# Optimization experiments

Measured on AMD Instinct MI355X. Metric: run time of the kernel, lower is better.

Reference implementation:

```python
import jax, jax.numpy as jnp
import numpy as np

NNK = 16
DENSITY_WEIGHT = 1.0


def _sq_dist(x, y):
    # x: [B, Nx, C], y: [B, Ny, C] -> [B, Nx, Ny] squared L2 distances.
    # Matmul form of the original broadcast-diff computation (same math,
    # avoids materializing [B, Nx, C, Ny]); clamp tiny negatives from fp error.
    x2 = jnp.sum(x * x, axis=-1)               # [B, Nx]
    y2 = jnp.sum(y * y, axis=-1)               # [B, Ny]
    xy = jnp.einsum('bnc,bmc->bnm', x, y)      # [B, Nx, Ny]
    return jnp.maximum(x2[:, :, None] + y2[:, None, :] - 2.0 * xy, 0.0)


def _safe_sqrt(s):
    # sqrt with zero (instead of inf) gradient at s == 0; forward values exact.
    pos = s > 0
    return jnp.where(pos, jnp.sqrt(jnp.where(pos, s, 1.0)), 0.0)


def setup_inputs() -> dict:
    key = jax.random.key(0)
    k1, k2 = jax.random.split(key)
    B, N, C = 2, 8192, 3
    y_pred = jax.random.normal(k1, (B, N, C), dtype=jnp.float32)
    y_true = jax.random.normal(k2, (B, N, C), dtype=jnp.float32)
    return {"y_pred": y_pred, "y_true": y_true}


def reference(y_pred, y_true):
    # dist[b, i, j] = || y_true[b, i] - y_pred[b, j] ||
    dist = _safe_sqrt(_sq_dist(y_true, y_pred))            # [B, Nt, Np]
    minrow = jnp.min(dist, axis=2)                         # per true point
    mincol = jnp.min(dist, axis=1)                         # per pred point
    shape_loss = (jnp.mean(minrow) + jnp.mean(mincol)) / 2

    dist2 = _safe_sqrt(_sq_dist(y_true, y_true))           # [B, Nt, Nt]
    knndis, _ = jax.lax.top_k(-dist, NNK)                  # [B, Nt, k]
    knndis2, _ = jax.lax.top_k(-dist2, NNK)                # [B, Nt, k]
    density_loss = jnp.mean(jnp.abs(knndis - knndis2))

    data_loss = shape_loss + density_loss * DENSITY_WEIGHT
    return (data_loss, shape_loss, density_loss)
```

## Files before the change

kernel.cpp:

```cpp
#include <hip/hip_runtime.h>
#include <math.h>

#define NPTS 8192
#define NB 2
#define NROWS (NB * NPTS)
#define KNN 16
#define KC 6

#define GRID 32
#define NCELLS (GRID * GRID * GRID)
#define TOTCELLS (4 * NCELLS)
#define H 0.35f
#define RLO (-5.6f)
#define INVH (1.0f / H)
#define SCAN_BLOCKS 128
#define SEGCAP 132

__device__ __forceinline__ int cellof(float x) {
  int c = (int)floorf((x - RLO) * INVH);
  return min(max(c, 0), GRID - 1);
}

__device__ __forceinline__ float sqd3(float qx, float qy, float qz, float4 c) {
  float dx = qx - c.x, dy = qy - c.y, dz = qz - c.z;
  return fmaf(dx, dx, fmaf(dy, dy, dz * dz));
}

__device__ __forceinline__ int lanerank(unsigned long long mk) {
  return __builtin_amdgcn_mbcnt_hi((unsigned)(mk >> 32),
                                   __builtin_amdgcn_mbcnt_lo((unsigned)mk, 0));
}

template <int K>
__device__ __forceinline__ void insertK(float (&a)[K], float d) {
  if (d < a[K - 1]) {
    a[K - 1] = d;
#pragma unroll
    for (int k = K - 1; k > 0; --k) {
      float lo = fminf(a[k - 1], a[k]);
      a[k] = fmaxf(a[k - 1], a[k]);
      a[k - 1] = lo;
    }
  }
}

__device__ __forceinline__ float bitonic_sort64(float v, int lane) {
#pragma unroll
  for (int k = 2; k <= 64; k <<= 1) {
#pragma unroll
    for (int j = k >> 1; j >= 1; j >>= 1) {
      float o = __shfl_xor(v, j, 64);
      bool up = ((lane & k) == 0);
      bool lower = ((lane & j) == 0);
      float mn = fminf(v, o), mx = fmaxf(v, o);
      v = (up == lower) ? mn : mx;
    }
  }
  return v;
}

template <int K, int NEED>
__device__ void wave_grid_knn(int g, float qx, float qy, float qz,
                              const float4* __restrict__ sorted,
                              const unsigned* __restrict__ pack,
                              unsigned* sS, unsigned* sC, unsigned* sPre,
                              int lane, float (&a)[K], float& dmin,
                              int& cnt, float& bnd2) {
  const int cx = cellof(qx), cy = cellof(qy), cz = cellof(qz);
  float fx = fminf(qx - (RLO + cx * H), (RLO + (cx + 1) * H) - qx);
  float fy = fminf(qy - (RLO + cy * H), (RLO + (cy + 1) * H) - qy);
  float fz = fminf(qz - (RLO + cz * H), (RLO + (cz + 1) * H) - qz);
  const float fq = fminf(fx, fminf(fy, fz));
  const int base = g * NCELLS;
  for (int m = 0; m <= GRID; ++m) {
    const int zlo = max(cz - m, 0), zhi = min(cz + m, GRID - 1);
    const int ylo = max(cy - m, 0), yhi = min(cy + m, GRID - 1);
    const int xlo = max(cx - m, 0), xhi = min(cx + m, GRID - 1);
    const int ny = yhi - ylo + 1;
    const int nrows = (zhi - zlo + 1) * ny;
    for (int rb = 0; rb < nrows; rb += 64) {
      const int rho = rb + lane;
      const bool act = rho < nrows;
      const int rr = act ? rho : 0;
      const int z = zlo + rr / ny, y = ylo + rr % ny;
      const int dza = abs(z - cz), dya = abs(y - cy);
      const bool bdry = (dza == m) || (dya == m);
      unsigned stA = 0, cnA = 0, stB = 0, cnB = 0;
      const int rowbase = base + (z * GRID + y) * GRID;
      if (act) {
        if (bdry) {
          unsigned plo = pack[rowbase + xlo];
          unsigned phi = pack[rowbase + xhi];
          stA = plo >> 14;
          cnA = ((phi >> 14) + (phi & 16383u)) - stA;
        } else {
          int xl = cx - m, xr = cx + m;
          if (xl >= 0) { unsigned p = pack[rowbase + xl]; stA = p >> 14; cnA = p & 16383u; }
          if (xr < GRID) { unsigned p = pack[rowbase + xr]; stB = p >> 14; cnB = p & 16383u; }
        }
      }
      unsigned long long mA = __ballot(cnA > 0);
      unsigned long long mB = __ballot(cnB > 0);
      int nA = __popcll(mA);
      int nseg = nA + __popcll(mB);
      if (nseg == 0) continue;
      int slA = lanerank(mA), slB = nA + lanerank(mB);
      if (cnA > 0) { sS[slA] = stA; sC[slA] = cnA; }
      if (cnB > 0) { sS[slB] = stB; sC[slB] = cnB; }
      unsigned total = 0;
      for (int h = 0; h < 2; ++h) {
        int sl = h * 64 + lane;
        unsigned v = (sl < nseg) ? sC[sl] : 0u;
        unsigned inc = v;
#pragma unroll
        for (int s2 = 1; s2 < 64; s2 <<= 1) {
          unsigned t = __shfl_up(inc, s2, 64);
          if (lane >= s2) inc += t;
        }
        if (sl < nseg) sPre[sl] = total + inc - v;
        total += __shfl(inc, 63, 64);
        if (nseg <= 64) break;
      }
      int sh0 = (nseg > 1) ? (1 << (31 - __clz(nseg - 1))) : 0;
      for (unsigned cb = 0; cb < total; cb += 64) {
        unsigned c = cb + (unsigned)lane;
        bool cact = c < total;
        unsigned cc = cact ? c : (total - 1);
        int lo = 0;
        for (int sh = sh0; sh; sh >>= 1) {
          int mid = lo + sh;
          if (mid < nseg && sPre[mid] <= cc) lo = mid;
        }
        float4 p = sorted[sS[lo] + (cc - sPre[lo])];
        float d = cact ? sqd3(qx, qy, qz, p) : INFINITY;
        dmin = fminf(dmin, fmaxf(d, a[K - 1]));
        insertK(a, d);
      }
    }
    float bnd = fmaxf((float)m * H + fq, 0.0f) * 0.999f;
    bnd2 = bnd * bnd;
    int c = 0;
#pragma unroll
    for (int k = 0; k < K; ++k) c += (a[k] <= bnd2) ? 1 : 0;
#pragma unroll
    for (int s2 = 1; s2 < 64; s2 <<= 1) c += __shfl_xor(c, s2, 64);
    cnt = c;
    bool covered = (zlo == 0 && zhi == GRID - 1 && ylo == 0 && yhi == GRID - 1 &&
                    xlo == 0 && xhi == GRID - 1);
    if (c >= NEED || covered) break;
  }
}

__global__ __launch_bounds__(256) void count_kernel(
    const float* __restrict__ yp, const float* __restrict__ yt,
    unsigned* __restrict__ counts, int* __restrict__ pflat,
    unsigned* __restrict__ prank) {
  int t = blockIdx.x * 256 + threadIdx.x;
  const float* src;
  int g;
  if (t < NROWS) { src = yp + 3 * t; g = 2 * (t >> 13); }
  else { int u = t - NROWS; src = yt + 3 * u; g = 2 * (u >> 13) + 1; }
  int flat = g * NCELLS + (cellof(src[2]) * GRID + cellof(src[1])) * GRID + cellof(src[0]);
  unsigned r = atomicAdd(&counts[flat], 1u);
  pflat[t] = flat;
  prank[t] = r;
}

__global__ __launch_bounds__(1024) void scan1_kernel(
    const unsigned* __restrict__ counts, unsigned* __restrict__ partial,
    unsigned* __restrict__ aux) {
  __shared__ unsigned ws[16];
  const int t = threadIdx.x, lane = t & 63, wave = t >> 6;
  const int tid = blockIdx.x * 1024 + t;
  unsigned v = counts[tid];
  unsigned inc = v;
#pragma unroll
  for (int off = 1; off < 64; off <<= 1) {
    unsigned u = __shfl_up(inc, off, 64);
    if (lane >= off) inc += u;
  }
  if (lane == 63) ws[wave] = inc;
  __syncthreads();
  unsigned wex = 0;
  if (wave == 0) {
    unsigned o = (lane < 16) ? ws[lane] : 0u;
    unsigned wi = o;
#pragma unroll
    for (int off = 1; off < 16; off <<= 1) {
      unsigned u = __shfl_up(wi, off, 64);
      if (lane >= off) wi += u;
    }
    if (lane < 16) ws[lane] = wi - o;
  }
  __syncthreads();
  wex = ws[wave];
  partial[tid] = wex + inc - v;
  if (t == 1023) aux[blockIdx.x] = wex + inc;
}

__global__ __launch_bounds__(1024) void pack_kernel(
    const unsigned* __restrict__ counts, const unsigned* __restrict__ partial,
    const unsigned* __restrict__ aux, unsigned* __restrict__ pack) {
  __shared__ unsigned sa[2];
  const int t = threadIdx.x;
  if (t < 128) {
    unsigned v = (t < (int)blockIdx.x) ? aux[t] : 0u;
#pragma unroll
    for (int s = 1; s < 64; s <<= 1) v += __shfl_xor(v, s, 64);
    if ((t & 63) == 0) sa[t >> 6] = v;
  }
  __syncthreads();
  unsigned base = sa[0] + sa[1];
  int i = blockIdx.x * 1024 + t;
  pack[i] = ((partial[i] + base) << 14) | counts[i];
}

__global__ __launch_bounds__(256) void scatter_kernel(
    const float* __restrict__ yp, const float* __restrict__ yt,
    const unsigned* __restrict__ pack, const int* __restrict__ pflat,
    const unsigned* __restrict__ prank, float4* __restrict__ sorted) {
  int t = blockIdx.x * 256 + threadIdx.x;
  const float* src;
  int row;
  if (t < NROWS) { row = t; src = yp + 3 * t; }
  else { row = t - NROWS; src = yt + 3 * row; }
  unsigned pos = (pack[pflat[t]] >> 14) + prank[t];
  sorted[pos] = make_float4(src[0], src[1], src[2], __int_as_float(row));
}

__global__ __launch_bounds__(256) void query_kernel(
    const float4* __restrict__ sorted, const unsigned* __restrict__ pack,
    float* __restrict__ knnP, float* __restrict__ knnT,
    float* __restrict__ mincol_arr, unsigned* __restrict__ flags) {
  __shared__ unsigned sb[4][3][SEGCAP];
  __shared__ float cbw[4][64];
  const int wave = threadIdx.x >> 6, lane = threadIdx.x & 63;
  const int wid = blockIdx.x * 4 + wave;
  const int type = wid >> 14;
  const int qid = wid & 16383;
  const int b = qid >> 13;
  const int src_g = (type == 2) ? 2 * b : 2 * b + 1;
  const int tgt_g = (type == 0) ? 2 * b : 2 * b + 1;
  float4 e = sorted[src_g * NPTS + (qid & (NPTS - 1))];
  const int row = __float_as_int(e.w);
  unsigned* sS = sb[wave][0];
  unsigned* sC = sb[wave][1];
  unsigned* sP = sb[wave][2];
  float* cbuf = cbw[wave];
  if (type < 2) {
    float a[KC];
#pragma unroll
    for (int k = 0; k < KC; ++k) a[k] = INFINITY;
    float dmin = INFINITY, bnd2;
    int cnt;
    wave_grid_knn<KC, KNN>(tgt_g, e.x, e.y, e.z, sorted, pack, sS, sC, sP,
                           lane, a, dmin, cnt, bnd2);
    float tau;
    if (cnt >= KNN && cnt <= 64) {
      tau = bnd2;
    } else {
      float slm = bitonic_sort64(a[0], lane);
      tau = __shfl(slm, 15, 64);
    }
    int tot = 0;
    int idx[KC];
#pragma unroll
    for (int k = 0; k < KC; ++k) {
      unsigned long long mk = __ballot(a[k] <= tau);
      idx[k] = tot + lanerank(mk);
      tot += __popcll(mk);
    }
#pragma unroll
    for (int k = 0; k < KC; ++k)
      if (a[k] <= tau && idx[k] < 64) cbuf[idx[k]] = a[k];
    float v = (lane < tot) ? cbuf[lane] : INFINITY;
    v = bitonic_sort64(v, lane);
    float f15 = __shfl(v, 15, 64);
    bool bad = (tot > 64) || (__ballot(dmin <= f15) != 0ull);
    float* dst = (type == 0) ? knnP : knnT;
    if (lane < KNN) dst[row * KNN + lane] = sqrtf(v);
    if (lane == 0) flags[type * NROWS + row] = bad ? 1u : 0u;
  } else {
    float a1[1] = {INFINITY};
    float dmin = INFINITY, bnd2;
    int cnt;
    wave_grid_knn<1, 1>(tgt_g, e.x, e.y, e.z, sorted, pack, sS, sC, sP,
                        lane, a1, dmin, cnt, bnd2);
    float v = a1[0];
#pragma unroll
    for (int s = 1; s < 64; s <<= 1) v = fminf(v, __shfl_xor(v, s, 64));
    if (lane == 0) mincol_arr[row] = sqrtf(v);
  }
}

__device__ float exact16_rowlist(const float4* __restrict__ base,
                                 float qx, float qy, float qz, int lane) {
  float a[KNN];
#pragma unroll
  for (int k = 0; k < KNN; ++k) a[k] = INFINITY;
  for (int s = 0; s < NPTS / 64; ++s) {
    float d = sqd3(qx, qy, qz, base[s * 64 + lane]);
    insertK(a, d);
  }
  float res = INFINITY;
#pragma unroll 1
  for (int r = 0; r < KNN; ++r) {
    float v = a[0];
    int idx = lane;
#pragma unroll
    for (int s = 1; s < 64; s <<= 1) {
      float ov = __shfl_xor(v, s, 64);
      int oi = __shfl_xor(idx, s, 64);
      bool take = (ov < v) || (ov == v && oi < idx);
      v = take ? ov : v;
      idx = take ? oi : idx;
    }
    if (lane == r) res = v;
    if (lane == idx) {
#pragma unroll
      for (int k = 0; k < KNN - 1; ++k) a[k] = a[k + 1];
      a[KNN - 1] = INFINITY;
    }
  }
  return res;
}

__global__ __launch_bounds__(256) void combine_kernel(
    const float* __restrict__ yt, const float4* __restrict__ sorted,
    const unsigned* __restrict__ flags, float* __restrict__ knnP,
    float* __restrict__ knnT, const float* __restrict__ mincol_arr,
    double* __restrict__ pd) {
  __shared__ double s1[256], s2[256], s3[256];
  const int t = threadIdx.x, lane = t & 63, wave = t >> 6;
  const int row0 = blockIdx.x * 256;
  const int rbase = row0 + wave * 64;
  unsigned f0 = flags[rbase + lane];
  unsigned f1 = flags[NROWS + rbase + lane];
  unsigned long long m0 = __ballot(f0 != 0u);
  unsigned long long m1 = __ballot(f1 != 0u);
  while (m0) {
    int rr = __ffsll(m0) - 1; m0 &= m0 - 1;
    int row = rbase + rr;
    int bb = row >> 13;
    const float* q = yt + 3 * row;
    float s = exact16_rowlist(sorted + (size_t)(2 * bb) * NPTS, q[0], q[1], q[2], lane);
    if (lane < KNN) knnP[row * KNN + lane] = sqrtf(s);
  }
  while (m1) {
    int rr = __ffsll(m1) - 1; m1 &= m1 - 1;
    int row = rbase + rr;
    int bb = row >> 13;
    const float* q = yt + 3 * row;
    float s = exact16_rowlist(sorted + (size_t)(2 * bb + 1) * NPTS, q[0], q[1], q[2], lane);
    if (lane < KNN) knnT[row * KNN + lane] = sqrtf(s);
  }
  __syncthreads();
  const int row = row0 + t;
  float s = 0.0f;
#pragma unroll
  for (int k = 0; k < KNN; ++k)
    s += fabsf(knnP[row * KNN + k] - knnT[row * KNN + k]);
  s1[t] = (double)knnP[row * KNN];
  s2[t] = (double)mincol_arr[row];
  s3[t] = (double)s;
  __syncthreads();
  for (int off = 128; off > 0; off >>= 1) {
    if (t < off) { s1[t] += s1[t + off]; s2[t] += s2[t + off]; s3[t] += s3[t + off]; }
    __syncthreads();
  }
  if (t == 0) {
    pd[blockIdx.x * 3 + 0] = s1[0];
    pd[blockIdx.x * 3 + 1] = s2[0];
    pd[blockIdx.x * 3 + 2] = s3[0];
  }
}

__global__ __launch_bounds__(64) void finalize_kernel(
    const double* __restrict__ pd, float* __restrict__ out) {
  const int t = threadIdx.x;
  double a = pd[t * 3], b = pd[t * 3 + 1], c = pd[t * 3 + 2];
#pragma unroll
  for (int s = 32; s >= 1; s >>= 1) {
    a += __shfl_down(a, s, 64);
    b += __shfl_down(b, s, 64);
    c += __shfl_down(c, s, 64);
  }
  if (t == 0) {
    double shape = 0.5 * (a + b) / (double)NROWS;
    double dens = c / ((double)NROWS * KNN);
    out[0] = (float)(shape + dens);
    out[1] = (float)shape;
    out[2] = (float)dens;
  }
}

extern "C" void kernel_launch(void* const* d_in, const int* in_sizes, int n_in,
                              void* d_out, int out_size, void* d_ws, size_t ws_size,
                              hipStream_t stream) {
  (void)in_sizes; (void)n_in; (void)out_size; (void)ws_size;
  const float* yp = (const float*)d_in[0];
  const float* yt = (const float*)d_in[1];
  char* w = (char*)d_ws;
  unsigned* counts  = (unsigned*)w;  w += TOTCELLS * 4;
  unsigned* partial = (unsigned*)w;  w += TOTCELLS * 4;
  unsigned* aux     = (unsigned*)w;  w += 512;
  unsigned* pack    = (unsigned*)w;  w += TOTCELLS * 4;
  int*      pflat   = (int*)w;       w += 2 * NROWS * 4;
  unsigned* prank   = (unsigned*)w;  w += 2 * NROWS * 4;
  float4*   sorted  = (float4*)w;    w += 2 * NROWS * 16;
  float*    knnP    = (float*)w;     w += NROWS * KNN * 4;
  float*    knnT    = (float*)w;     w += NROWS * KNN * 4;
  float*    mincol  = (float*)w;     w += NROWS * 4;
  unsigned* flags   = (unsigned*)w;  w += 2 * NROWS * 4;
  double*   pd      = (double*)w;    w += 64 * 3 * 8;
  float* out = (float*)d_out;

  hipMemsetAsync(counts, 0, (size_t)TOTCELLS * 4, stream);
  count_kernel<<<2 * NROWS / 256, 256, 0, stream>>>(yp, yt, counts, pflat, prank);
  scan1_kernel<<<SCAN_BLOCKS, 1024, 0, stream>>>(counts, partial, aux);
  pack_kernel<<<SCAN_BLOCKS, 1024, 0, stream>>>(counts, partial, aux, pack);
  scatter_kernel<<<2 * NROWS / 256, 256, 0, stream>>>(yp, yt, pack, pflat, prank, sorted);
  query_kernel<<<3 * 16384 / 4, 256, 0, stream>>>(sorted, pack, knnP, knnT, mincol, flags);
  combine_kernel<<<64, 256, 0, stream>>>(yt, sorted, flags, knnP, knnT, mincol, pd);
  finalize_kernel<<<1, 64, 0, stream>>>(pd, out);
}
```

Measured before the change: 136.3 us.

## Share grid neighbor-cell gathering across query chunks within the same cell

```diff
diff --git a/kernel.cpp b/kernel.cpp
--- a/kernel.cpp
+++ b/kernel.cpp
@@ -16,6 +16,11 @@
 #define SCAN_BLOCKS 128
 #define SEGCAP 132
 
+#define QC 8
+#define CAP 1024
+#define NEED 192
+#define MAXCHUNK 8192
+
 __device__ __forceinline__ int cellof(float x) {
   int c = (int)floorf((x - RLO) * INVH);
   return min(max(c, 0), GRID - 1);
@@ -59,26 +64,136 @@
   return v;
 }
 
-template <int K, int NEED>
-__device__ void wave_grid_knn(int g, float qx, float qy, float qz,
-                              const float4* __restrict__ sorted,
-                              const unsigned* __restrict__ pack,
-                              unsigned* sS, unsigned* sC, unsigned* sPre,
-                              int lane, float (&a)[K], float& dmin,
-                              int& cnt, float& bnd2) {
-  const int cx = cellof(qx), cy = cellof(qy), cz = cellof(qz);
-  float fx = fminf(qx - (RLO + cx * H), (RLO + (cx + 1) * H) - qx);
-  float fy = fminf(qy - (RLO + cy * H), (RLO + (cy + 1) * H) - qy);
-  float fz = fminf(qz - (RLO + cz * H), (RLO + (cz + 1) * H) - qz);
-  const float fq = fminf(fx, fminf(fy, fz));
-  const int base = g * NCELLS;
+__global__ __launch_bounds__(256) void count_kernel(
+    const float* __restrict__ yp, const float* __restrict__ yt,
+    unsigned* __restrict__ counts, int* __restrict__ pflat,
+    unsigned* __restrict__ prank, unsigned* __restrict__ wcnt) {
+  if (blockIdx.x == 0 && threadIdx.x < 4) wcnt[threadIdx.x] = 0;
+  int t = blockIdx.x * 256 + threadIdx.x;
+  const float* src;
+  int g;
+  if (t < NROWS) { src = yp + 3 * t; g = 2 * (t >> 13); }
+  else { int u = t - NROWS; src = yt + 3 * u; g = 2 * (u >> 13) + 1; }
+  int flat = g * NCELLS + (cellof(src[2]) * GRID + cellof(src[1])) * GRID + cellof(src[0]);
+  unsigned r = atomicAdd(&counts[flat], 1u);
+  pflat[t] = flat;
+  prank[t] = r;
+}
+
+__global__ __launch_bounds__(1024) void scan1_kernel(
+    const unsigned* __restrict__ counts, unsigned* __restrict__ partial,
+    unsigned* __restrict__ aux) {
+  __shared__ unsigned ws[16];
+  const int t = threadIdx.x, lane = t & 63, wave = t >> 6;
+  const int tid = blockIdx.x * 1024 + t;
+  unsigned v = counts[tid];
+  unsigned inc = v;
+#pragma unroll
+  for (int off = 1; off < 64; off <<= 1) {
+    unsigned u = __shfl_up(inc, off, 64);
+    if (lane >= off) inc += u;
+  }
+  if (lane == 63) ws[wave] = inc;
+  __syncthreads();
+  unsigned wex = 0;
+  if (wave == 0) {
+    unsigned o = (lane < 16) ? ws[lane] : 0u;
+    unsigned wi = o;
+#pragma unroll
+    for (int off = 1; off < 16; off <<= 1) {
+      unsigned u = __shfl_up(wi, off, 64);
+      if (lane >= off) wi += u;
+    }
+    if (lane < 16) ws[lane] = wi - o;
+  }
+  __syncthreads();
+  wex = ws[wave];
+  partial[tid] = wex + inc - v;
+  if (t == 1023) aux[blockIdx.x] = wex + inc;
+}
+
+__global__ __launch_bounds__(1024) void pack_kernel(
+    const unsigned* __restrict__ counts, const unsigned* __restrict__ partial,
+    const unsigned* __restrict__ aux, unsigned* __restrict__ pack,
+    unsigned* __restrict__ wcnt, unsigned* __restrict__ wlist) {
+  __shared__ unsigned sa[2];
+  const int t = threadIdx.x;
+  if (t < 128) {
+    unsigned v = (t < (int)blockIdx.x) ? aux[t] : 0u;
+#pragma unroll
+    for (int s = 1; s < 64; s <<= 1) v += __shfl_xor(v, s, 64);
+    if ((t & 63) == 0) sa[t >> 6] = v;
+  }
+  __syncthreads();
+  unsigned base = sa[0] + sa[1];
+  int i = blockIdx.x * 1024 + t;
+  unsigned cnti = counts[i];
+  pack[i] = ((partial[i] + base) << 14) | cnti;
+  if (cnti > 0) {
+    int g = i >> 15;
+    unsigned cellw = (unsigned)(i & (NCELLS - 1));
+    unsigned nch = (cnti + QC - 1) / QC;
+    unsigned slot = atomicAdd(&wcnt[g], nch);
+    for (unsigned j = 0; j < nch; ++j)
+      wlist[g * MAXCHUNK + slot + j] = (cellw << 11) | j;
+  }
+}
+
+__global__ __launch_bounds__(256) void scatter_kernel(
+    const float* __restrict__ yp, const float* __restrict__ yt,
+    const unsigned* __restrict__ pack, const int* __restrict__ pflat,
+    const unsigned* __restrict__ prank, float4* __restrict__ sorted) {
+  int t = blockIdx.x * 256 + threadIdx.x;
+  const float* src;
+  int row;
+  if (t < NROWS) { row = t; src = yp + 3 * t; }
+  else { row = t - NROWS; src = yt + 3 * row; }
+  unsigned pos = (pack[pflat[t]] >> 14) + prank[t];
+  sorted[pos] = make_float4(src[0], src[1], src[2], __int_as_float(row));
+}
+
+__global__ __launch_bounds__(256) void query_kernel(
+    const float4* __restrict__ sorted, const unsigned* __restrict__ pack,
+    const unsigned* __restrict__ wcnt, const unsigned* __restrict__ wlist,
+    float* __restrict__ knnP, float* __restrict__ knnT,
+    float* __restrict__ mincol_arr, unsigned* __restrict__ flags) {
+  __shared__ unsigned sb[4][3][SEGCAP];
+  __shared__ unsigned short bufw[4][CAP];
+  __shared__ float4 qbw[4][QC];
+  __shared__ float cbw[4][64];
+  const int wave = threadIdx.x >> 6, lane = threadIdx.x & 63;
+  const int wid = blockIdx.x * 4 + wave;
+  const int seg = wid >> 13;
+  const int idx = wid & 8191;
+  const int b = seg / 3, task = seg % 3;
+  const int qg = (task == 2) ? 2 * b : 2 * b + 1;
+  const int tg = (task == 0) ? 2 * b : 2 * b + 1;
+  if ((unsigned)idx >= wcnt[qg]) return;
+  const unsigned e = wlist[qg * MAXCHUNK + idx];
+  const int cell = (int)(e >> 11);
+  const int qoff = (int)(e & 2047u) * QC;
+  const unsigned pc = pack[qg * NCELLS + cell];
+  const int cstart = (int)(pc >> 14);
+  const int ccnt = (int)(pc & 16383u);
+  const int nq = min(QC, ccnt - qoff);
+  if (lane < nq) qbw[wave][lane] = sorted[cstart + qoff + lane];
+  const int cx = cell & (GRID - 1), cy = (cell >> 5) & (GRID - 1), cz = cell >> 10;
+  unsigned* sS = sb[wave][0];
+  unsigned* sC = sb[wave][1];
+  unsigned* sP = sb[wave][2];
+  unsigned short* buf = bufw[wave];
+  float* cbuf = cbw[wave];
+
+  int bufcount = 0, M = 0;
+  bool overflow = false;
+  const int base = tg * NCELLS;
   for (int m = 0; m <= GRID; ++m) {
     const int zlo = max(cz - m, 0), zhi = min(cz + m, GRID - 1);
     const int ylo = max(cy - m, 0), yhi = min(cy + m, GRID - 1);
     const int xlo = max(cx - m, 0), xhi = min(cx + m, GRID - 1);
     const int ny = yhi - ylo + 1;
     const int nrows = (zhi - zlo + 1) * ny;
-    for (int rb = 0; rb < nrows; rb += 64) {
+    for (int rb = 0; rb < nrows && !overflow; rb += 64) {
       const int rho = rb + lane;
       const bool act = rho < nrows;
       const int rr = act ? rho : 0;
@@ -117,179 +232,108 @@
           unsigned t = __shfl_up(inc, s2, 64);
           if (lane >= s2) inc += t;
         }
-        if (sl < nseg) sPre[sl] = total + inc - v;
+        if (sl < nseg) sP[sl] = total + inc - v;
         total += __shfl(inc, 63, 64);
         if (nseg <= 64) break;
       }
       int sh0 = (nseg > 1) ? (1 << (31 - __clz(nseg - 1))) : 0;
       for (unsigned cb = 0; cb < total; cb += 64) {
         unsigned c = cb + (unsigned)lane;
-        bool cact = c < total;
-        unsigned cc = cact ? c : (total - 1);
-        int lo = 0;
-        for (int sh = sh0; sh; sh >>= 1) {
-          int mid = lo + sh;
-          if (mid < nseg && sPre[mid] <= cc) lo = mid;
+        if (c < total && (int)c + bufcount < CAP) {
+          int lo = 0;
+          for (int sh = sh0; sh; sh >>= 1) {
+            int mid = lo + sh;
+            if (mid < nseg && sP[mid] <= c) lo = mid;
+          }
+          buf[bufcount + (int)c] = (unsigned short)(sS[lo] + (c - sP[lo]));
         }
-        float4 p = sorted[sS[lo] + (cc - sPre[lo])];
-        float d = cact ? sqd3(qx, qy, qz, p) : INFINITY;
-        dmin = fminf(dmin, fmaxf(d, a[K - 1]));
-        insertK(a, d);
-      }
-    }
-    float bnd = fmaxf((float)m * H + fq, 0.0f) * 0.999f;
-    bnd2 = bnd * bnd;
-    int c = 0;
-#pragma unroll
-    for (int k = 0; k < K; ++k) c += (a[k] <= bnd2) ? 1 : 0;
-#pragma unroll
-    for (int s2 = 1; s2 < 64; s2 <<= 1) c += __shfl_xor(c, s2, 64);
-    cnt = c;
+      }
+      bufcount += (int)total;
+      if (bufcount > CAP) overflow = true;
+    }
+    if (overflow) break;
+    M = m;
     bool covered = (zlo == 0 && zhi == GRID - 1 && ylo == 0 && yhi == GRID - 1 &&
                     xlo == 0 && xhi == GRID - 1);
-    if (c >= NEED || covered) break;
-  }
-}
-
-__global__ __launch_bounds__(256) void count_kernel(
-    const float* __restrict__ yp, const float* __restrict__ yt,
-    unsigned* __restrict__ counts, int* __restrict__ pflat,
-    unsigned* __restrict__ prank) {
-  int t = blockIdx.x * 256 + threadIdx.x;
-  const float* src;
-  int g;
-  if (t < NROWS) { src = yp + 3 * t; g = 2 * (t >> 13); }
-  else { int u = t - NROWS; src = yt + 3 * u; g = 2 * (u >> 13) + 1; }
-  int flat = g * NCELLS + (cellof(src[2]) * GRID + cellof(src[1])) * GRID + cellof(src[0]);
-  unsigned r = atomicAdd(&counts[flat], 1u);
-  pflat[t] = flat;
-  prank[t] = r;
-}
-
-__global__ __launch_bounds__(1024) void scan1_kernel(
-    const unsigned* __restrict__ counts, unsigned* __restrict__ partial,
-    unsigned* __restrict__ aux) {
-  __shared__ unsigned ws[16];
-  const int t = threadIdx.x, lane = t & 63, wave = t >> 6;
-  const int tid = blockIdx.x * 1024 + t;
-  unsigned v = counts[tid];
-  unsigned inc = v;
-#pragma unroll
-  for (int off = 1; off < 64; off <<= 1) {
-    unsigned u = __shfl_up(inc, off, 64);
-    if (lane >= off) inc += u;
-  }
-  if (lane == 63) ws[wave] = inc;
-  __syncthreads();
-  unsigned wex = 0;
-  if (wave == 0) {
-    unsigned o = (lane < 16) ? ws[lane] : 0u;
-    unsigned wi = o;
-#pragma unroll
-    for (int off = 1; off < 16; off <<= 1) {
-      unsigned u = __shfl_up(wi, off, 64);
-      if (lane >= off) wi += u;
-    }
-    if (lane < 16) ws[lane] = wi - o;
-  }
-  __syncthreads();
-  wex = ws[wave];
-  partial[tid] = wex + inc - v;
-  if (t == 1023) aux[blockIdx.x] = wex + inc;
-}
-
-__global__ __launch_bounds__(1024) void pack_kernel(
-    const unsigned* __restrict__ counts, const unsigned* __restrict__ partial,
-    const unsigned* __restrict__ aux, unsigned* __restrict__ pack) {
-  __shared__ unsigned sa[2];
-  const int t = threadIdx.x;
-  if (t < 128) {
-    unsigned v = (t < (int)blockIdx.x) ? aux[t] : 0u;
-#pragma unroll
-    for (int s = 1; s < 64; s <<= 1) v += __shfl_xor(v, s, 64);
-    if ((t & 63) == 0) sa[t >> 6] = v;
-  }
-  __syncthreads();
-  unsigned base = sa[0] + sa[1];
-  int i = blockIdx.x * 1024 + t;
-  pack[i] = ((partial[i] + base) << 14) | counts[i];
-}
-
-__global__ __launch_bounds__(256) void scatter_kernel(
-    const float* __restrict__ yp, const float* __restrict__ yt,
-    const unsigned* __restrict__ pack, const int* __restrict__ pflat,
-    const unsigned* __restrict__ prank, float4* __restrict__ sorted) {
-  int t = blockIdx.x * 256 + threadIdx.x;
-  const float* src;
-  int row;
-  if (t < NROWS) { row = t; src = yp + 3 * t; }
-  else { row = t - NROWS; src = yt + 3 * row; }
-  unsigned pos = (pack[pflat[t]] >> 14) + prank[t];
-  sorted[pos] = make_float4(src[0], src[1], src[2], __int_as_float(row));
-}
-
-__global__ __launch_bounds__(256) void query_kernel(
-    const float4* __restrict__ sorted, const unsigned* __restrict__ pack,
-    float* __restrict__ knnP, float* __restrict__ knnT,
-    float* __restrict__ mincol_arr, unsigned* __restrict__ flags) {
-  __shared__ unsigned sb[4][3][SEGCAP];
-  __shared__ float cbw[4][64];
-  const int wave = threadIdx.x >> 6, lane = threadIdx.x & 63;
-  const int wid = blockIdx.x * 4 + wave;
-  const int type = wid >> 14;
-  const int qid = wid & 16383;
-  const int b = qid >> 13;
-  const int src_g = (type == 2) ? 2 * b : 2 * b + 1;
-  const int tgt_g = (type == 0) ? 2 * b : 2 * b + 1;
-  float4 e = sorted[src_g * NPTS + (qid & (NPTS - 1))];
-  const int row = __float_as_int(e.w);
-  unsigned* sS = sb[wave][0];
-  unsigned* sC = sb[wave][1];
-  unsigned* sP = sb[wave][2];
-  float* cbuf = cbw[wave];
-  if (type < 2) {
-    float a[KC];
-#pragma unroll
-    for (int k = 0; k < KC; ++k) a[k] = INFINITY;
-    float dmin = INFINITY, bnd2;
-    int cnt;
-    wave_grid_knn<KC, KNN>(tgt_g, e.x, e.y, e.z, sorted, pack, sS, sC, sP,
-                           lane, a, dmin, cnt, bnd2);
-    float tau;
-    if (cnt >= KNN && cnt <= 64) {
-      tau = bnd2;
+    if (covered || (m >= 1 && bufcount >= NEED)) break;
+  }
+
+  const float mh = (float)M * H;
+  for (int j = 0; j < nq; ++j) {
+    float4 q = qbw[wave][j];
+    const int row = __float_as_int(q.w);
+    float fx = fminf(q.x - (RLO + cx * H), (RLO + (cx + 1) * H) - q.x);
+    float fy = fminf(q.y - (RLO + cy * H), (RLO + (cy + 1) * H) - q.y);
+    float fz = fminf(q.z - (RLO + cz * H), (RLO + (cz + 1) * H) - q.z);
+    float fq = fminf(fx, fminf(fy, fz));
+    float bnd = fmaxf(mh + fq, 0.0f) * 0.999f;
+    float bnd2 = bnd * bnd;
+    if (task < 2) {
+      float a[KC];
+#pragma unroll
+      for (int k = 0; k < KC; ++k) a[k] = INFINITY;
+      float dmin = INFINITY;
+      bool act = lane < bufcount;
+      float4 p = sorted[act ? (int)buf[lane] : 0];
+      for (int cb = 0; cb < bufcount; cb += 64) {
+        int pos2 = cb + 64 + lane;
+        bool act2 = pos2 < bufcount;
+        float4 p2 = sorted[act2 ? (int)buf[pos2] : 0];
+        float d = act ? sqd3(q.x, q.y, q.z, p) : INFINITY;
+        dmin = fminf(dmin, fmaxf(d, a[KC - 1]));
+        insertK(a, d);
+        p = p2; act = act2;
+      }
+      int cntq = 0;
+#pragma unroll
+      for (int k = 0; k < KC; ++k) cntq += (a[k] <= bnd2) ? 1 : 0;
+#pragma unroll
+      for (int s2 = 1; s2 < 64; s2 <<= 1) cntq += __shfl_xor(cntq, s2, 64);
+      float tau;
+      if (cntq >= KNN && cntq <= 64) {
+        tau = bnd2;
+      } else {
+        float slm = bitonic_sort64(a[0], lane);
+        tau = __shfl(slm, 15, 64);
+      }
+      int tot = 0;
+      int idxk[KC];
+#pragma unroll
+      for (int k = 0; k < KC; ++k) {
+        unsigned long long mk = __ballot(a[k] <= tau);
+        idxk[k] = tot + lanerank(mk);
+        tot += __popcll(mk);
+      }
+#pragma unroll
+      for (int k = 0; k < KC; ++k)
+        if (a[k] <= tau && idxk[k] < 64) cbuf[idxk[k]] = a[k];
+      float v = (lane < tot) ? cbuf[lane] : INFINITY;
+      v = bitonic_sort64(v, lane);
+      float f15 = __shfl(v, 15, 64);
+      bool bad = overflow || (tot > 64) || (__ballot(dmin <= f15) != 0ull) ||
+                 (f15 > bnd2);
+      float* dst = (task == 0) ? knnP : knnT;
+      if (lane < KNN) dst[row * KNN + lane] = sqrtf(v);
+      if (lane == 0) flags[task * NROWS + row] = bad ? 1u : 0u;
     } else {
-      float slm = bitonic_sort64(a[0], lane);
-      tau = __shfl(slm, 15, 64);
-    }
-    int tot = 0;
-    int idx[KC];
-#pragma unroll
-    for (int k = 0; k < KC; ++k) {
-      unsigned long long mk = __ballot(a[k] <= tau);
-      idx[k] = tot + lanerank(mk);
-      tot += __popcll(mk);
-    }
-#pragma unroll
-    for (int k = 0; k < KC; ++k)
-      if (a[k] <= tau && idx[k] < 64) cbuf[idx[k]] = a[k];
-    float v = (lane < tot) ? cbuf[lane] : INFINITY;
-    v = bitonic_sort64(v, lane);
-    float f15 = __shfl(v, 15, 64);
-    bool bad = (tot > 64) || (__ballot(dmin <= f15) != 0ull);
-    float* dst = (type == 0) ? knnP : knnT;
-    if (lane < KNN) dst[row * KNN + lane] = sqrtf(v);
-    if (lane == 0) flags[type * NROWS + row] = bad ? 1u : 0u;
-  } else {
-    float a1[1] = {INFINITY};
-    float dmin = INFINITY, bnd2;
-    int cnt;
-    wave_grid_knn<1, 1>(tgt_g, e.x, e.y, e.z, sorted, pack, sS, sC, sP,
-                        lane, a1, dmin, cnt, bnd2);
-    float v = a1[0];
-#pragma unroll
-    for (int s = 1; s < 64; s <<= 1) v = fminf(v, __shfl_xor(v, s, 64));
-    if (lane == 0) mincol_arr[row] = sqrtf(v);
+      float v = INFINITY;
+      bool act = lane < bufcount;
+      float4 p = sorted[act ? (int)buf[lane] : 0];
+      for (int cb = 0; cb < bufcount; cb += 64) {
+        int pos2 = cb + 64 + lane;
+        bool act2 = pos2 < bufcount;
+        float4 p2 = sorted[act2 ? (int)buf[pos2] : 0];
+        if (act) v = fminf(v, sqd3(q.x, q.y, q.z, p));
+        p = p2; act = act2;
+      }
+#pragma unroll
+      for (int s2 = 1; s2 < 64; s2 <<= 1) v = fminf(v, __shfl_xor(v, s2, 64));
+      bool bad = overflow || (v > bnd2);
+      if (lane == 0) {
+        mincol_arr[row] = sqrtf(v);
+        flags[2 * NROWS + row] = bad ? 1u : 0u;
+      }
+    }
   }
 }
 
@@ -326,18 +370,20 @@
 }
 
 __global__ __launch_bounds__(256) void combine_kernel(
-    const float* __restrict__ yt, const float4* __restrict__ sorted,
-    const unsigned* __restrict__ flags, float* __restrict__ knnP,
-    float* __restrict__ knnT, const float* __restrict__ mincol_arr,
-    double* __restrict__ pd) {
+    const float* __restrict__ yp, const float* __restrict__ yt,
+    const float4* __restrict__ sorted, const unsigned* __restrict__ flags,
+    float* __restrict__ knnP, float* __restrict__ knnT,
+    float* __restrict__ mincol_arr, double* __restrict__ pd) {
   __shared__ double s1[256], s2[256], s3[256];
   const int t = threadIdx.x, lane = t & 63, wave = t >> 6;
   const int row0 = blockIdx.x * 256;
   const int rbase = row0 + wave * 64;
   unsigned f0 = flags[rbase + lane];
   unsigned f1 = flags[NROWS + rbase + lane];
+  unsigned f2 = flags[2 * NROWS + rbase + lane];
   unsigned long long m0 = __ballot(f0 != 0u);
   unsigned long long m1 = __ballot(f1 != 0u);
+  unsigned long long m2 = __ballot(f2 != 0u);
   while (m0) {
     int rr = __ffsll(m0) - 1; m0 &= m0 - 1;
     int row = rbase + rr;
@@ -353,6 +399,19 @@
     const float* q = yt + 3 * row;
     float s = exact16_rowlist(sorted + (size_t)(2 * bb + 1) * NPTS, q[0], q[1], q[2], lane);
     if (lane < KNN) knnT[row * KNN + lane] = sqrtf(s);
+  }
+  while (m2) {
+    int rr = __ffsll(m2) - 1; m2 &= m2 - 1;
+    int row = rbase + rr;
+    int bb = row >> 13;
+    const float* q = yp + 3 * row;
+    const float4* bp = sorted + (size_t)(2 * bb + 1) * NPTS;
+    float v = INFINITY;
+    for (int s = 0; s < NPTS / 64; ++s)
+      v = fminf(v, sqd3(q[0], q[1], q[2], bp[s * 64 + lane]));
+#pragma unroll
+    for (int s = 1; s < 64; s <<= 1) v = fminf(v, __shfl_xor(v, s, 64));
+    if (lane == 0) mincol_arr[row] = sqrtf(v);
   }
   __syncthreads();
   const int row = row0 + t;
@@ -411,16 +470,19 @@
   float*    knnP    = (float*)w;     w += NROWS * KNN * 4;
   float*    knnT    = (float*)w;     w += NROWS * KNN * 4;
   float*    mincol  = (float*)w;     w += NROWS * 4;
-  unsigned* flags   = (unsigned*)w;  w += 2 * NROWS * 4;
+  unsigned* flags   = (unsigned*)w;  w += 3 * NROWS * 4;
   double*   pd      = (double*)w;    w += 64 * 3 * 8;
+  unsigned* wcnt    = (unsigned*)w;  w += 64;
+  unsigned* wlist   = (unsigned*)w;  w += 4 * MAXCHUNK * 4;
   float* out = (float*)d_out;
 
   hipMemsetAsync(counts, 0, (size_t)TOTCELLS * 4, stream);
-  count_kernel<<<2 * NROWS / 256, 256, 0, stream>>>(yp, yt, counts, pflat, prank);
+  count_kernel<<<2 * NROWS / 256, 256, 0, stream>>>(yp, yt, counts, pflat, prank, wcnt);
   scan1_kernel<<<SCAN_BLOCKS, 1024, 0, stream>>>(counts, partial, aux);
-  pack_kernel<<<SCAN_BLOCKS, 1024, 0, stream>>>(counts, partial, aux, pack);
+  pack_kernel<<<SCAN_BLOCKS, 1024, 0, stream>>>(counts, partial, aux, pack, wcnt, wlist);
   scatter_kernel<<<2 * NROWS / 256, 256, 0, stream>>>(yp, yt, pack, pflat, prank, sorted);
-  query_kernel<<<3 * 16384 / 4, 256, 0, stream>>>(sorted, pack, knnP, knnT, mincol, flags);
-  combine_kernel<<<64, 256, 0, stream>>>(yt, sorted, flags, knnP, knnT, mincol, pd);
+  query_kernel<<<6 * 8192 / 4, 256, 0, stream>>>(sorted, pack, wcnt, wlist,
+                                                 knnP, knnT, mincol, flags);
+  combine_kernel<<<64, 256, 0, stream>>>(yp, yt, sorted, flags, knnP, knnT, mincol, pd);
   finalize_kernel<<<1, 64, 0, stream>>>(pd, out);
 }
```

Result: slower. 239.9 us (+75.9%).

## Batch up to three same-cell queries per wave via a cell-based work list

Applied to the files above, without the earlier changes.

```diff
diff --git a/kernel.cpp b/kernel.cpp
--- a/kernel.cpp
+++ b/kernel.cpp
@@ -16,6 +16,10 @@
 #define SCAN_BLOCKS 128
 #define SEGCAP 132
 
+#define QC 3
+#define WLCAP 49152
+#define QBLOCKS 2048
+
 __device__ __forceinline__ int cellof(float x) {
   int c = (int)floorf((x - RLO) * INVH);
   return min(max(c, 0), GRID - 1);
@@ -59,18 +63,22 @@
   return v;
 }
 
-template <int K, int NEED>
-__device__ void wave_grid_knn(int g, float qx, float qy, float qz,
-                              const float4* __restrict__ sorted,
-                              const unsigned* __restrict__ pack,
-                              unsigned* sS, unsigned* sC, unsigned* sPre,
-                              int lane, float (&a)[K], float& dmin,
-                              int& cnt, float& bnd2) {
-  const int cx = cellof(qx), cy = cellof(qy), cz = cellof(qz);
-  float fx = fminf(qx - (RLO + cx * H), (RLO + (cx + 1) * H) - qx);
-  float fy = fminf(qy - (RLO + cy * H), (RLO + (cy + 1) * H) - qy);
-  float fz = fminf(qz - (RLO + cz * H), (RLO + (cz + 1) * H) - qz);
-  const float fq = fminf(fx, fminf(fy, fz));
+template <int K, int NEEDQ>
+__device__ __forceinline__ void wave_grid_knn_q(
+    int g, int cx, int cy, int cz,
+    const float (&qx)[QC], const float (&qy)[QC], const float (&qz)[QC],
+    const float4* __restrict__ sorted, const unsigned* __restrict__ pack,
+    unsigned* sS, unsigned* sC, unsigned* sPre, int lane,
+    float (&a)[QC][K], float (&dminq)[QC], int (&cntq)[QC],
+    float (&bnd2q)[QC]) {
+  float fq[QC];
+#pragma unroll
+  for (int q = 0; q < QC; ++q) {
+    float fx = fminf(qx[q] - (RLO + cx * H), (RLO + (cx + 1) * H) - qx[q]);
+    float fy = fminf(qy[q] - (RLO + cy * H), (RLO + (cy + 1) * H) - qy[q]);
+    float fz = fminf(qz[q] - (RLO + cz * H), (RLO + (cz + 1) * H) - qz[q]);
+    fq[q] = fminf(fx, fminf(fy, fz));
+  }
   const int base = g * NCELLS;
   for (int m = 0; m <= GRID; ++m) {
     const int zlo = max(cz - m, 0), zhi = min(cz + m, GRID - 1);
@@ -132,29 +140,45 @@
           if (mid < nseg && sPre[mid] <= cc) lo = mid;
         }
         float4 p = sorted[sS[lo] + (cc - sPre[lo])];
-        float d = cact ? sqd3(qx, qy, qz, p) : INFINITY;
-        dmin = fminf(dmin, fmaxf(d, a[K - 1]));
-        insertK(a, d);
-      }
-    }
-    float bnd = fmaxf((float)m * H + fq, 0.0f) * 0.999f;
-    bnd2 = bnd * bnd;
-    int c = 0;
-#pragma unroll
-    for (int k = 0; k < K; ++k) c += (a[k] <= bnd2) ? 1 : 0;
-#pragma unroll
-    for (int s2 = 1; s2 < 64; s2 <<= 1) c += __shfl_xor(c, s2, 64);
-    cnt = c;
+#pragma unroll
+        for (int q = 0; q < QC; ++q) {
+          float d = cact ? sqd3(qx[q], qy[q], qz[q], p) : INFINITY;
+          dminq[q] = fminf(dminq[q], fmaxf(d, a[q][K - 1]));
+          insertK(a[q], d);
+        }
+      }
+    }
+#pragma unroll
+    for (int q = 0; q < QC; ++q) {
+      float bnd = fmaxf((float)m * H + fq[q], 0.0f) * 0.999f;
+      bnd2q[q] = bnd * bnd;
+    }
+    int cpA = 0, cpB = 0;
+#pragma unroll
+    for (int k = 0; k < K; ++k) {
+      cpA += (a[0][k] <= bnd2q[0] ? 1 : 0) + (a[1][k] <= bnd2q[1] ? 65536 : 0);
+      cpB += (a[2][k] <= bnd2q[2] ? 1 : 0);
+    }
+#pragma unroll
+    for (int s2 = 1; s2 < 64; s2 <<= 1) {
+      cpA += __shfl_xor(cpA, s2, 64);
+      cpB += __shfl_xor(cpB, s2, 64);
+    }
+    cntq[0] = cpA & 0xffff;
+    cntq[1] = cpA >> 16;
+    cntq[2] = cpB;
+    bool okall = (cntq[0] >= NEEDQ) && (cntq[1] >= NEEDQ) && (cntq[2] >= NEEDQ);
     bool covered = (zlo == 0 && zhi == GRID - 1 && ylo == 0 && yhi == GRID - 1 &&
                     xlo == 0 && xhi == GRID - 1);
-    if (c >= NEED || covered) break;
+    if (okall || covered) break;
   }
 }
 
 __global__ __launch_bounds__(256) void count_kernel(
     const float* __restrict__ yp, const float* __restrict__ yt,
     unsigned* __restrict__ counts, int* __restrict__ pflat,
-    unsigned* __restrict__ prank) {
+    unsigned* __restrict__ prank, unsigned* __restrict__ wcnt) {
+  if (blockIdx.x == 0 && threadIdx.x < 8) wcnt[threadIdx.x] = 0;
   int t = blockIdx.x * 256 + threadIdx.x;
   const float* src;
   int g;
@@ -200,7 +224,8 @@
 
 __global__ __launch_bounds__(1024) void pack_kernel(
     const unsigned* __restrict__ counts, const unsigned* __restrict__ partial,
-    const unsigned* __restrict__ aux, unsigned* __restrict__ pack) {
+    const unsigned* __restrict__ aux, unsigned* __restrict__ pack,
+    unsigned* __restrict__ wcnt, unsigned* __restrict__ wlist) {
   __shared__ unsigned sa[2];
   const int t = threadIdx.x;
   if (t < 128) {
@@ -212,7 +237,25 @@
   __syncthreads();
   unsigned base = sa[0] + sa[1];
   int i = blockIdx.x * 1024 + t;
-  pack[i] = ((partial[i] + base) << 14) | counts[i];
+  unsigned cnti = counts[i];
+  pack[i] = ((partial[i] + base) << 14) | cnti;
+  if (cnti > 0) {
+    int g = i >> 15;
+    unsigned b = (unsigned)(g >> 1);
+    unsigned cellw = (unsigned)(i & (NCELLS - 1));
+    unsigned nch = (cnti + QC - 1) / QC;
+    if (g & 1) {
+      unsigned slot = atomicAdd(&wcnt[4], 2 * nch);
+      for (unsigned j = 0; j < nch; ++j) {
+        wlist[slot + 2 * j]     = (b << 30) | (0u << 28) | (cellw << 13) | j;
+        wlist[slot + 2 * j + 1] = (b << 30) | (1u << 28) | (cellw << 13) | j;
+      }
+    } else {
+      unsigned slot = atomicAdd(&wcnt[4], nch);
+      for (unsigned j = 0; j < nch; ++j)
+        wlist[slot + j] = (b << 30) | (2u << 28) | (cellw << 13) | j;
+    }
+  }
 }
 
 __global__ __launch_bounds__(256) void scatter_kernel(
@@ -230,66 +273,101 @@
 
 __global__ __launch_bounds__(256) void query_kernel(
     const float4* __restrict__ sorted, const unsigned* __restrict__ pack,
+    const unsigned* __restrict__ wcnt, const unsigned* __restrict__ wlist,
     float* __restrict__ knnP, float* __restrict__ knnT,
     float* __restrict__ mincol_arr, unsigned* __restrict__ flags) {
   __shared__ unsigned sb[4][3][SEGCAP];
   __shared__ float cbw[4][64];
   const int wave = threadIdx.x >> 6, lane = threadIdx.x & 63;
-  const int wid = blockIdx.x * 4 + wave;
-  const int type = wid >> 14;
-  const int qid = wid & 16383;
-  const int b = qid >> 13;
-  const int src_g = (type == 2) ? 2 * b : 2 * b + 1;
-  const int tgt_g = (type == 0) ? 2 * b : 2 * b + 1;
-  float4 e = sorted[src_g * NPTS + (qid & (NPTS - 1))];
-  const int row = __float_as_int(e.w);
   unsigned* sS = sb[wave][0];
   unsigned* sC = sb[wave][1];
   unsigned* sP = sb[wave][2];
   float* cbuf = cbw[wave];
-  if (type < 2) {
-    float a[KC];
-#pragma unroll
-    for (int k = 0; k < KC; ++k) a[k] = INFINITY;
-    float dmin = INFINITY, bnd2;
-    int cnt;
-    wave_grid_knn<KC, KNN>(tgt_g, e.x, e.y, e.z, sorted, pack, sS, sC, sP,
-                           lane, a, dmin, cnt, bnd2);
-    float tau;
-    if (cnt >= KNN && cnt <= 64) {
-      tau = bnd2;
+  const unsigned nwork = wcnt[4];
+  const unsigned nw = gridDim.x * 4;
+  for (unsigned wrk = blockIdx.x * 4 + wave; wrk < nwork; wrk += nw) {
+    const unsigned e = wlist[wrk];
+    const int b = (int)((e >> 30) & 1u);
+    const int task = (int)((e >> 28) & 3u);
+    const int cell = (int)((e >> 13) & 32767u);
+    const int qoff = (int)(e & 8191u) * QC;
+    const int qg = (task == 2) ? 2 * b : 2 * b + 1;
+    const int tg = (task == 0) ? 2 * b : 2 * b + 1;
+    const unsigned pc = pack[qg * NCELLS + cell];
+    const int cstart = (int)(pc >> 14);
+    const int ccnt = (int)(pc & 16383u);
+    const int nq = min(QC, ccnt - qoff);
+    const int cx = cell & (GRID - 1), cy = (cell >> 5) & (GRID - 1), cz = cell >> 10;
+
+    float qx[QC], qy[QC], qz[QC];
+    int rowq[QC];
+#pragma unroll
+    for (int q = 0; q < QC; ++q) {
+      float4 eq = sorted[cstart + qoff + min(q, nq - 1)];
+      qx[q] = eq.x; qy[q] = eq.y; qz[q] = eq.z;
+      rowq[q] = __float_as_int(eq.w);
+    }
+
+    if (task < 2) {
+      float a[QC][KC];
+      float dminq[QC];
+#pragma unroll
+      for (int q = 0; q < QC; ++q) {
+        dminq[q] = INFINITY;
+#pragma unroll
+        for (int k = 0; k < KC; ++k) a[q][k] = INFINITY;
+      }
+      int cntq[QC];
+      float bnd2q[QC];
+      wave_grid_knn_q<KC, KNN>(tg, cx, cy, cz, qx, qy, qz, sorted, pack,
+                               sS, sC, sP, lane, a, dminq, cntq, bnd2q);
+      float* dstbase = (task == 0) ? knnP : knnT;
+#pragma unroll
+      for (int q = 0; q < QC; ++q) {
+        if (q >= nq) break;
+        float tau;
+        if (cntq[q] >= KNN && cntq[q] <= 64) {
+          tau = bnd2q[q];
+        } else {
+          float slm = bitonic_sort64(a[q][0], lane);
+          tau = __shfl(slm, 15, 64);
+        }
+        int tot = 0;
+        int idxk[KC];
+#pragma unroll
+        for (int k = 0; k < KC; ++k) {
+          unsigned long long mk = __ballot(a[q][k] <= tau);
+          idxk[k] = tot + lanerank(mk);
+          tot += __popcll(mk);
+        }
+#pragma unroll
+        for (int k = 0; k < KC; ++k)
+          if (a[q][k] <= tau && idxk[k] < 64) cbuf[idxk[k]] = a[q][k];
+        float v = (lane < tot) ? cbuf[lane] : INFINITY;
+        v = bitonic_sort64(v, lane);
+        float f15 = __shfl(v, 15, 64);
+        bool bad = (tot > 64) || (__ballot(dminq[q] <= f15) != 0ull);
+        if (lane < KNN) dstbase[rowq[q] * KNN + lane] = sqrtf(v);
+        if (lane == 0) flags[task * NROWS + rowq[q]] = bad ? 1u : 0u;
+      }
     } else {
-      float slm = bitonic_sort64(a[0], lane);
-      tau = __shfl(slm, 15, 64);
-    }
-    int tot = 0;
-    int idx[KC];
-#pragma unroll
-    for (int k = 0; k < KC; ++k) {
-      unsigned long long mk = __ballot(a[k] <= tau);
-      idx[k] = tot + lanerank(mk);
-      tot += __popcll(mk);
-    }
-#pragma unroll
-    for (int k = 0; k < KC; ++k)
-      if (a[k] <= tau && idx[k] < 64) cbuf[idx[k]] = a[k];
-    float v = (lane < tot) ? cbuf[lane] : INFINITY;
-    v = bitonic_sort64(v, lane);
-    float f15 = __shfl(v, 15, 64);
-    bool bad = (tot > 64) || (__ballot(dmin <= f15) != 0ull);
-    float* dst = (type == 0) ? knnP : knnT;
-    if (lane < KNN) dst[row * KNN + lane] = sqrtf(v);
-    if (lane == 0) flags[type * NROWS + row] = bad ? 1u : 0u;
-  } else {
-    float a1[1] = {INFINITY};
-    float dmin = INFINITY, bnd2;
-    int cnt;
-    wave_grid_knn<1, 1>(tgt_g, e.x, e.y, e.z, sorted, pack, sS, sC, sP,
-                        lane, a1, dmin, cnt, bnd2);
-    float v = a1[0];
-#pragma unroll
-    for (int s = 1; s < 64; s <<= 1) v = fminf(v, __shfl_xor(v, s, 64));
-    if (lane == 0) mincol_arr[row] = sqrtf(v);
+      float a1[QC][1];
+      float dminq[QC];
+#pragma unroll
+      for (int q = 0; q < QC; ++q) { a1[q][0] = INFINITY; dminq[q] = INFINITY; }
+      int cntq[QC];
+      float bnd2q[QC];
+      wave_grid_knn_q<1, 1>(tg, cx, cy, cz, qx, qy, qz, sorted, pack,
+                            sS, sC, sP, lane, a1, dminq, cntq, bnd2q);
+#pragma unroll
+      for (int q = 0; q < QC; ++q) {
+        if (q >= nq) break;
+        float v = a1[q][0];
+#pragma unroll
+        for (int s2 = 1; s2 < 64; s2 <<= 1) v = fminf(v, __shfl_xor(v, s2, 64));
+        if (lane == 0) mincol_arr[rowq[q]] = sqrtf(v);
+      }
+    }
   }
 }
 
@@ -413,14 +491,17 @@
   float*    mincol  = (float*)w;     w += NROWS * 4;
   unsigned* flags   = (unsigned*)w;  w += 2 * NROWS * 4;
   double*   pd      = (double*)w;    w += 64 * 3 * 8;
+  unsigned* wcnt    = (unsigned*)w;  w += 64;
+  unsigned* wlist   = (unsigned*)w;  w += WLCAP * 4;
   float* out = (float*)d_out;
 
   hipMemsetAsync(counts, 0, (size_t)TOTCELLS * 4, stream);
-  count_kernel<<<2 * NROWS / 256, 256, 0, stream>>>(yp, yt, counts, pflat, prank);
+  count_kernel<<<2 * NROWS / 256, 256, 0, stream>>>(yp, yt, counts, pflat, prank, wcnt);
   scan1_kernel<<<SCAN_BLOCKS, 1024, 0, stream>>>(counts, partial, aux);
-  pack_kernel<<<SCAN_BLOCKS, 1024, 0, stream>>>(counts, partial, aux, pack);
+  pack_kernel<<<SCAN_BLOCKS, 1024, 0, stream>>>(counts, partial, aux, pack, wcnt, wlist);
   scatter_kernel<<<2 * NROWS / 256, 256, 0, stream>>>(yp, yt, pack, pflat, prank, sorted);
-  query_kernel<<<3 * 16384 / 4, 256, 0, stream>>>(sorted, pack, knnP, knnT, mincol, flags);
+  query_kernel<<<QBLOCKS, 256, 0, stream>>>(sorted, pack, wcnt, wlist,
+                                            knnP, knnT, mincol, flags);
   combine_kernel<<<64, 256, 0, stream>>>(yt, sorted, flags, knnP, knnT, mincol, pd);
   finalize_kernel<<<1, 64, 0, stream>>>(pd, out);
 }
```

After: 154.5 us. 13.4% more time.
